# Optimization experiments

Hardware: AMD Instinct MI355X
Metric: run time of the kernel (lower is better)

Reference implementation:

```python
import jax, jax.numpy as jnp
import numpy as np

D_MODEL, SEQ, D_HEAD, N_HEAD, D_MLP = 1024, 2048, 64, 16, 4096
BATCH = 2
LN_EPS = 1e-5


def layer_norm(x, gamma, beta):
    mu = jnp.mean(x, axis=-1, keepdims=True)
    var = jnp.mean(jnp.square(x - mu), axis=-1, keepdims=True)
    return (x - mu) * jax.lax.rsqrt(var + LN_EPS) * gamma + beta


def setup_inputs() -> dict:
    key = jax.random.key(0)
    ks = jax.random.split(key, 10)
    s = 1.0 / np.sqrt(D_MODEL)
    x = jax.random.normal(ks[0], (BATCH, SEQ, D_MODEL), dtype=jnp.float32)
    # per-head Q/K/V projections, stacked: [H, d_model, d_head]
    wq = jax.random.uniform(ks[1], (N_HEAD, D_MODEL, D_HEAD), jnp.float32, -s, s)
    wk = jax.random.uniform(ks[2], (N_HEAD, D_MODEL, D_HEAD), jnp.float32, -s, s)
    wv = jax.random.uniform(ks[3], (N_HEAD, D_MODEL, D_HEAD), jnp.float32, -s, s)
    wo = jax.random.uniform(ks[4], (N_HEAD * D_HEAD, D_MODEL), jnp.float32, -s, s)
    sm = 1.0 / np.sqrt(D_MLP)
    w_in = jax.random.uniform(ks[5], (D_MODEL, D_MLP), jnp.float32, -s, s)
    b_in = jax.random.uniform(ks[6], (D_MLP,), jnp.float32, -s, s)
    w_out = jax.random.uniform(ks[7], (D_MLP, D_MODEL), jnp.float32, -sm, sm)
    b_out = jax.random.uniform(ks[8], (D_MODEL,), jnp.float32, -sm, sm)
    g1 = jnp.ones((D_MODEL,), jnp.float32)
    bt1 = jnp.zeros((D_MODEL,), jnp.float32)
    g2 = jnp.ones((D_MODEL,), jnp.float32)
    bt2 = jnp.zeros((D_MODEL,), jnp.float32)
    return {"x": x, "wq": wq, "wk": wk, "wv": wv, "wo": wo,
            "w_in": w_in, "b_in": b_in, "w_out": w_out, "b_out": b_out,
            "g1": g1, "bt1": bt1, "g2": g2, "bt2": bt2}


def reference(x, wq, wk, wv, wo, w_in, b_in, w_out, b_out, g1, bt1, g2, bt2):
    B, S, D = x.shape
    # multi-head attention (all heads batched)
    q = jnp.einsum('bsd,hde->bhse', x, wq)  # [B,H,S,dh]
    k = jnp.einsum('bsd,hde->bhse', x, wk)
    v = jnp.einsum('bsd,hde->bhse', x, wv)
    scores = jnp.einsum('bhie,bhje->bhij', q, k) / np.sqrt(D_HEAD)
    causal = jnp.tril(jnp.ones((S, S), dtype=bool))
    scores = jnp.where(causal, scores, -jnp.inf)
    attn = jax.nn.softmax(scores, axis=-1)
    head_out = jnp.einsum('bhij,bhje->bhie', attn, v)  # [B,H,S,dh]
    # concat heads in order (head 0 first) -> [B,S,H*dh]
    head_out = jnp.transpose(head_out, (0, 2, 1, 3)).reshape(B, S, N_HEAD * D_HEAD)
    x = x + layer_norm(head_out @ wo, g1, bt1)
    mlp = jax.nn.relu(x @ w_in + b_in) @ w_out + b_out
    x = x + layer_norm(mlp, g2, bt2)
    return x
```

## Files before the change

kernel.cpp:

```cpp
#include <hip/hip_runtime.h>
#include <hip/hip_bf16.h>
#include <math.h>

#define DM 1024
#define SEQ 2048
#define DH 64
#define NH 16
#define DMLP 4096
#define BATCH 2
#define ROWS (BATCH*SEQ)

typedef __attribute__((ext_vector_type(4))) float f32x4;
typedef __attribute__((ext_vector_type(8))) short bf16x8;

__device__ __forceinline__ void gl2lds16(const __hip_bfloat16* g, __hip_bfloat16* l) {
  __builtin_amdgcn_global_load_lds(
      (const __attribute__((address_space(1))) void*)g,
      (__attribute__((address_space(3))) void*)l, 16, 0, 0);
}

__device__ __forceinline__ float bfu2f(unsigned short u) {
  union { unsigned int i; float f; } cvt;
  cvt.i = ((unsigned int)u) << 16;
  return cvt.f;
}

template<int K, int OUT_BF16, int BIAS, int RELU>
__global__ __launch_bounds__(512) void gemm256(
    const __hip_bfloat16* __restrict__ A,
    const __hip_bfloat16* __restrict__ BT,
    float* __restrict__ Cf,
    __hip_bfloat16* __restrict__ Cb,
    const float* __restrict__ bias,
    int N)
{
  constexpr int NT = K / 64;
  __shared__ __align__(16) __hip_bfloat16 As[2][16384];
  __shared__ __align__(16) __hip_bfloat16 Bs[2][16384];
  const int t    = threadIdx.x;
  const int wave = t >> 6;
  const int lane = t & 63;
  const int col  = lane & 15;
  const int quad = lane >> 4;
  const int m0 = blockIdx.x * 256;
  const int n0 = blockIdx.y * 256;
  const int wm = (wave >> 2) * 128;
  const int wn = (wave & 3) * 64;

  const int tr = t >> 3;
  const int tc = (t & 7) ^ (tr & 7);
  const __hip_bfloat16* gA = A  + (size_t)(m0 + tr) * K + tc * 8;
  const __hip_bfloat16* gB = BT + (size_t)(n0 + tr) * K + tc * 8;

  const int sw  = col & 7;
  const int ao0 = ((quad)     ^ sw) * 8;
  const int ao1 = ((4 + quad) ^ sw) * 8;

  f32x4 acc[8][4] = {};

#define STAGE_A(h, u) do {                                                     \
    gl2lds16(gA + (size_t)(h)*128*K + (u)*64,                                  \
             &As[(u)&1][(h)*8192 + wave*512]);                                 \
    gl2lds16(gA + (size_t)(h)*128*K + (u)*64 + (size_t)64*K,                   \
             &As[(u)&1][(h)*8192 + 4096 + wave*512]);                          \
  } while (0)
#define STAGE_B(h, u) do {                                                     \
    gl2lds16(gB + (size_t)(h)*128*K + (u)*64,                                  \
             &Bs[(u)&1][(h)*8192 + wave*512]);                                 \
    gl2lds16(gB + (size_t)(h)*128*K + (u)*64 + (size_t)64*K,                   \
             &Bs[(u)&1][(h)*8192 + 4096 + wave*512]);                          \
  } while (0)
#define LOAD_A(base) do { _Pragma("unroll")                                    \
    for (int i = 0; i < 4; ++i) {                                              \
      af[i][0] = *(const bf16x8*)(pA + (base) + i*1024 + ao0);                 \
      af[i][1] = *(const bf16x8*)(pA + (base) + i*1024 + ao1);                 \
    } } while (0)
#define LOAD_BX(arr, base) do { _Pragma("unroll")                              \
    for (int j = 0; j < 2; ++j) {                                              \
      arr[j][0] = *(const bf16x8*)(pB + (base) + j*1024 + ao0);                \
      arr[j][1] = *(const bf16x8*)(pB + (base) + j*1024 + ao1);                \
    } } while (0)
#define PHASE_TAIL(MB, NB, BARR) do {                                          \
    asm volatile("s_barrier" ::: "memory");                                    \
    asm volatile("s_waitcnt lgkmcnt(0)" ::: "memory");                         \
    __builtin_amdgcn_s_setprio(1);                                             \
    _Pragma("unroll")                                                          \
    for (int kk = 0; kk < 2; ++kk)                                             \
      _Pragma("unroll")                                                        \
      for (int i = 0; i < 4; ++i)                                              \
        _Pragma("unroll")                                                      \
        for (int j = 0; j < 2; ++j)                                            \
          acc[(MB)+i][(NB)+j] = __builtin_amdgcn_mfma_f32_16x16x32_bf16(       \
              af[i][kk], BARR[j][kk], acc[(MB)+i][(NB)+j], 0, 0, 0);           \
    __builtin_amdgcn_s_setprio(0);                                             \
    asm volatile("s_barrier" ::: "memory");                                    \
  } while (0)

  STAGE_A(0, 0); STAGE_B(0, 0); STAGE_A(1, 0); STAGE_B(1, 0);
  if (NT > 1) {
    STAGE_A(0, 1); STAGE_B(0, 1); STAGE_A(1, 1); STAGE_B(1, 1);
    asm volatile("s_waitcnt vmcnt(8)" ::: "memory");
  } else {
    asm volatile("s_waitcnt vmcnt(0)" ::: "memory");
  }
  asm volatile("s_barrier" ::: "memory");

  #pragma unroll 2
  for (int u = 0; u < NT; ++u) {
    const __hip_bfloat16* pA = As[u & 1] + (wm + col) * 64;
    const __hip_bfloat16* pB = Bs[u & 1] + (wn + col) * 64;
    const bool s2 = (u + 2 < NT);
    bf16x8 af[4][2], bl[2][2], bh[2][2];

    LOAD_A(0);
    LOAD_BX(bl, 0);
    PHASE_TAIL(0, 0, bl);

    LOAD_BX(bh, 2048);
    PHASE_TAIL(0, 2, bh);

    LOAD_A(4096);
    if (s2) { STAGE_B(0, u + 2); STAGE_B(1, u + 2); }
    PHASE_TAIL(4, 2, bh);

    if (s2) {
      STAGE_A(0, u + 2); STAGE_A(1, u + 2);
      asm volatile("s_waitcnt vmcnt(8)" ::: "memory");
    } else {
      asm volatile("s_waitcnt vmcnt(0)" ::: "memory");
    }
    PHASE_TAIL(4, 0, bl);
  }
#undef STAGE_A
#undef STAGE_B
#undef LOAD_A
#undef LOAD_BX
#undef PHASE_TAIL

  #pragma unroll
  for (int mi = 0; mi < 8; ++mi) {
    #pragma unroll
    for (int ni = 0; ni < 4; ++ni) {
      const int cn = n0 + wn + ni*16 + col;
      float bv = 0.f;
      if (BIAS) bv = bias[cn];
      #pragma unroll
      for (int r = 0; r < 4; ++r) {
        const int cm = m0 + wm + mi*16 + quad*4 + r;
        float v = acc[mi][ni][r];
        if (BIAS) v += bv;
        if (RELU) v = fmaxf(v, 0.f);
        if (OUT_BF16) Cb[(size_t)cm * N + cn] = __float2bfloat16(v);
        else          Cf[(size_t)cm * N + cn] = v;
      }
    }
  }
}

template<int KS>
__global__ __launch_bounds__(512) void gemm256x128(
    const __hip_bfloat16* __restrict__ A,
    const __hip_bfloat16* __restrict__ BT,
    float* __restrict__ Cf,
    int N, int K, long long zstride)
{
  constexpr int NT = KS / 64;
  static_assert(NT >= 2, "pipeline needs >=2 K-tiles");
  __shared__ __align__(16) __hip_bfloat16 As[2][16384];
  __shared__ __align__(16) __hip_bfloat16 Bs[2][8192];
  const int t    = threadIdx.x;
  const int wave = t >> 6;
  const int lane = t & 63;
  const int col  = lane & 15;
  const int quad = lane >> 4;
  const int m0 = blockIdx.x * 256;
  const int n0 = blockIdx.y * 128;
  const int kz = (int)blockIdx.z * KS;
  const int wm = (wave >> 1) * 64;
  const int wn = (wave & 1) * 64;

  const int tr = t >> 3;
  const int tc = (t & 7) ^ (tr & 7);
  const __hip_bfloat16* gA = A  + (size_t)(m0 + tr) * K + kz + tc * 8;
  const __hip_bfloat16* gB = BT + (size_t)(n0 + tr) * K + kz + tc * 8;

  const int sw  = col & 7;
  const int ao0 = ((quad)     ^ sw) * 8;
  const int ao1 = ((4 + quad) ^ sw) * 8;

  f32x4 acc[4][4] = {};

#define SA(u) do { _Pragma("unroll")                                           \
    for (int q = 0; q < 4; ++q)                                                \
      gl2lds16(gA + (size_t)(q*64)*K + (u)*64,                                 \
               &As[(u)&1][q*4096 + wave*512]);                                 \
  } while (0)
#define SB(u) do { _Pragma("unroll")                                           \
    for (int q = 0; q < 2; ++q)                                                \
      gl2lds16(gB + (size_t)(q*64)*K + (u)*64,                                 \
               &Bs[(u)&1][q*4096 + wave*512]);                                 \
  } while (0)

  SA(0); SB(0); SA(1);

  #pragma unroll 2
  for (int v = 0; v < NT; ++v) {
    const __hip_bfloat16* pA = As[v & 1] + (wm + col) * 64;
    const __hip_bfloat16* pB = Bs[v & 1] + (wn + col) * 64;
    bf16x8 af[4][2], bf[4][2];

    if (v + 1 < NT) {
      SB(v + 1);
      asm volatile("s_waitcnt vmcnt(6)" ::: "memory");
    } else {
      asm volatile("s_waitcnt vmcnt(0)" ::: "memory");
    }
    asm volatile("s_barrier" ::: "memory");
    #pragma unroll
    for (int i = 0; i < 4; ++i) {
      af[i][0] = *(const bf16x8*)(pA + i*1024 + ao0);
      af[i][1] = *(const bf16x8*)(pA + i*1024 + ao1);
    }
    #pragma unroll
    for (int j = 0; j < 2; ++j) {
      bf[j][0] = *(const bf16x8*)(pB + j*1024 + ao0);
      bf[j][1] = *(const bf16x8*)(pB + j*1024 + ao1);
    }
    asm volatile("s_waitcnt lgkmcnt(0)" ::: "memory");
    __builtin_amdgcn_s_setprio(1);
    #pragma unroll
    for (int kk = 0; kk < 2; ++kk)
      #pragma unroll
      for (int i = 0; i < 4; ++i)
        #pragma unroll
        for (int j = 0; j < 2; ++j)
          acc[i][j] = __builtin_amdgcn_mfma_f32_16x16x32_bf16(
              af[i][kk], bf[j][kk], acc[i][j], 0, 0, 0);
    __builtin_amdgcn_s_setprio(0);
    asm volatile("s_barrier" ::: "memory");

    if (v + 2 < NT) SA(v + 2);
    #pragma unroll
    for (int j = 2; j < 4; ++j) {
      bf[j][0] = *(const bf16x8*)(pB + j*1024 + ao0);
      bf[j][1] = *(const bf16x8*)(pB + j*1024 + ao1);
    }
    asm volatile("s_waitcnt lgkmcnt(0)" ::: "memory");
    __builtin_amdgcn_s_setprio(1);
    #pragma unroll
    for (int kk = 0; kk < 2; ++kk)
      #pragma unroll
      for (int i = 0; i < 4; ++i)
        #pragma unroll
        for (int j = 2; j < 4; ++j)
          acc[i][j] = __builtin_amdgcn_mfma_f32_16x16x32_bf16(
              af[i][kk], bf[j][kk], acc[i][j], 0, 0, 0);
    __builtin_amdgcn_s_setprio(0);
    asm volatile("s_barrier" ::: "memory");
  }
#undef SA
#undef SB

  float* Co = Cf + (size_t)blockIdx.z * zstride;
  #pragma unroll
  for (int i = 0; i < 4; ++i) {
    #pragma unroll
    for (int j = 0; j < 4; ++j) {
      const int cn = n0 + wn + j*16 + col;
      #pragma unroll
      for (int r = 0; r < 4; ++r) {
        const int cm = m0 + wm + i*16 + quad*4 + r;
        Co[(size_t)cm * N + cn] = acc[i][j][r];
      }
    }
  }
}

__global__ __launch_bounds__(256) void attn_kernel(
    const __hip_bfloat16* __restrict__ qkv,
    const __hip_bfloat16* __restrict__ vt,
    __hip_bfloat16* __restrict__ aout,
    __hip_bfloat16* __restrict__ opart,
    float* __restrict__ lpart)
{
  __shared__ __align__(16) __hip_bfloat16 Ks[2][64*64];
  __shared__ __align__(16) __hip_bfloat16 Vts[2][64*64];
  __shared__ __align__(16) __hip_bfloat16 Ps[4][16*64];

  const int bh = blockIdx.x, b = bh >> 4, h = bh & 15;
  const int t = threadIdx.x, wave = t >> 6, lane = t & 63;
  const int col = lane & 15, quad = lane >> 4;
  const float SC = 0.125f * 1.44269504f;

  const int r0  = t >> 3;
  const int cs0 = (t & 7) ^ (r0 & 7);
  const __hip_bfloat16* kbase = qkv + (size_t)b*SEQ*3072 + 1024 + h*64;
  const __hip_bfloat16* vbase = vt + (size_t)bh*64*SEQ;

#define KISSUE(j0, buf) do {                                                      \
    gl2lds16(kbase + (size_t)((j0) + r0)*3072      + cs0*8, &Ks[buf][wave*512]);  \
    gl2lds16(kbase + (size_t)((j0) + 32 + r0)*3072 + cs0*8, &Ks[buf][2048 + wave*512]); \
  } while (0)
#define VISSUE(j0, buf) do {                                                      \
    gl2lds16(vbase + (size_t)r0*SEQ        + (j0) + cs0*8,  &Vts[buf][wave*512]); \
    gl2lds16(vbase + (size_t)(32 + r0)*SEQ + (j0) + cs0*8,  &Vts[buf][2048 + wave*512]); \
  } while (0)

  const int y = (int)blockIdx.y;
  int c, tile;
  if (y < 32)      { c = 0; tile = 31 - y;  }
  else if (y < 56) { c = 1; tile = 63 - y;  }
  else if (y < 72) { c = 2; tile = 87 - y;  }
  else             { c = 3; tile = 103 - y; }
  const int jbeg = c * 8;
  const int jend = jbeg + min(8, tile + 1 - jbeg);

  const int i0 = tile * 64;
  const int i0w = i0 + wave*16;

  bf16x8 aq[2];
  #pragma unroll
  for (int kk = 0; kk < 2; kk++)
    aq[kk] = *(const bf16x8*)&qkv[((size_t)(b*SEQ + i0w + col))*3072 + h*64 + kk*32 + quad*8];

  f32x4 O[4] = {};
  float lsum[4] = {0.f, 0.f, 0.f, 0.f};

  KISSUE(jbeg * 64, 0);
  VISSUE(jbeg * 64, 0);
  for (int jt = jbeg; jt < jend; jt++) {
    const int cur = (jt - jbeg) & 1;
    const int j0 = jt * 64;
    const bool pf = (jt + 1 < jend);
    asm volatile("s_barrier" ::: "memory");
    if (pf) {
      KISSUE(j0 + 64, cur ^ 1);
      VISSUE(j0 + 64, cur ^ 1);
      asm volatile("s_waitcnt vmcnt(4)" ::: "memory");
    } else {
      asm volatile("s_waitcnt vmcnt(0)" ::: "memory");
    }

    f32x4 S[4] = {};
    __builtin_amdgcn_s_setprio(1);
    #pragma unroll
    for (int kk = 0; kk < 2; kk++) {
      const int sl = ((kk*4 + quad) ^ (col & 7)) * 8;
      #pragma unroll
      for (int jl = 0; jl < 4; jl++) {
        bf16x8 bk = *(const bf16x8*)&Ks[cur][(jl*16 + col)*64 + sl];
        S[jl] = __builtin_amdgcn_mfma_f32_16x16x32_bf16(aq[kk], bk, S[jl], 0, 0, 0);
      }
    }
    __builtin_amdgcn_s_setprio(0);

    if (jt == tile) {
      #pragma unroll
      for (int r = 0; r < 4; r++) {
        const int row = quad*4 + r;
        const int ig = i0 + wave*16 + row;
        #pragma unroll
        for (int jl = 0; jl < 4; jl++) {
          float p = __builtin_amdgcn_exp2f(S[jl][r] * SC);
          if (j0 + jl*16 + col > ig) p = 0.f;
          lsum[r] += p;
          const int cc = jl*2 + (col >> 3);
          Ps[wave][row*64 + (cc ^ (row & 7))*8 + (col & 7)] = __float2bfloat16(p);
        }
      }
    } else {
      #pragma unroll
      for (int r = 0; r < 4; r++) {
        const int row = quad*4 + r;
        #pragma unroll
        for (int jl = 0; jl < 4; jl++) {
          float p = __builtin_amdgcn_exp2f(S[jl][r] * SC);
          lsum[r] += p;
          const int cc = jl*2 + (col >> 3);
          Ps[wave][row*64 + (cc ^ (row & 7))*8 + (col & 7)] = __float2bfloat16(p);
        }
      }
    }

    __builtin_amdgcn_s_setprio(1);
    #pragma unroll
    for (int kk = 0; kk < 2; kk++) {
      const int sl = ((kk*4 + quad) ^ (col & 7)) * 8;
      bf16x8 ap = *(const bf16x8*)&Ps[wave][col*64 + sl];
      #pragma unroll
      for (int et = 0; et < 4; et++) {
        bf16x8 bv = *(const bf16x8*)&Vts[cur][(et*16 + col)*64 + sl];
        O[et] = __builtin_amdgcn_mfma_f32_16x16x32_bf16(ap, bv, O[et], 0, 0, 0);
      }
    }
    __builtin_amdgcn_s_setprio(0);
  }

  #pragma unroll
  for (int r = 0; r < 4; r++) {
    float s = lsum[r];
    s += __shfl_xor(s, 1);
    s += __shfl_xor(s, 2);
    s += __shfl_xor(s, 4);
    s += __shfl_xor(s, 8);
    const int m = b*SEQ + i0w + quad*4 + r;
    if (tile < 8) {
      const float inv = __builtin_amdgcn_rcpf(s);
      #pragma unroll
      for (int et = 0; et < 4; et++)
        aout[(size_t)m*DM + h*64 + et*16 + col] = __float2bfloat16(O[et][r] * inv);
    } else {
      __hip_bfloat16* op = opart + ((size_t)c*ROWS + m)*DM + h*64;
      #pragma unroll
      for (int et = 0; et < 4; et++)
        op[et*16 + col] = __float2bfloat16(O[et][r]);
      if (col == 0) lpart[((size_t)c*ROWS + m)*16 + h] = s;
    }
  }
#undef KISSUE
#undef VISSUE
}

__global__ __launch_bounds__(256) void attn_finalize(
    const __hip_bfloat16* __restrict__ opart,
    const float* __restrict__ lpart,
    __hip_bfloat16* __restrict__ aout)
{
  const int y = blockIdx.x;
  const int b = y / 1536;
  const int rem = y % 1536;
  const int tile = 8 + (rem >> 6);
  const int rr = rem & 63;
  const int m = b*SEQ + tile*64 + rr;
  const int nch = (tile >> 3) + 1;
  const int tid = threadIdx.x;
  const int h = tid >> 4;
  float o0 = 0.f, o1 = 0.f, o2 = 0.f, o3 = 0.f, l = 0.f;
  for (int c = 0; c < nch; ++c) {
    const ushort4 v = ((const ushort4*)(opart + ((size_t)c*ROWS + m)*DM))[tid];
    o0 += bfu2f(v.x); o1 += bfu2f(v.y); o2 += bfu2f(v.z); o3 += bfu2f(v.w);
    l  += lpart[((size_t)c*ROWS + m)*16 + h];
  }
  const float inv = __builtin_amdgcn_rcpf(l);
  __hip_bfloat16* p = aout + (size_t)m*DM + tid*4;
  p[0] = __float2bfloat16(o0 * inv);
  p[1] = __float2bfloat16(o1 * inv);
  p[2] = __float2bfloat16(o2 * inv);
  p[3] = __float2bfloat16(o3 * inv);
}

__global__ __launch_bounds__(256) void ln_res(
    const float* __restrict__ y0,
    const float* __restrict__ y1,
    const float* __restrict__ bias,
    const float* __restrict__ xres,
    float* __restrict__ xout,
    __hip_bfloat16* __restrict__ bout,
    const float* __restrict__ gamma,
    const float* __restrict__ beta)
{
  const int row = blockIdx.x;
  const int t = threadIdx.x;
  float4 v = ((const float4*)(y0 + (size_t)row*DM))[t];
  if (y1) {
    const float4 w = ((const float4*)(y1 + (size_t)row*DM))[t];
    v.x += w.x; v.y += w.y; v.z += w.z; v.w += w.w;
  }
  if (bias) {
    const float4 w = ((const float4*)bias)[t];
    v.x += w.x; v.y += w.y; v.z += w.z; v.w += w.w;
  }
  float s  = v.x + v.y + v.z + v.w;
  float sq = v.x*v.x + v.y*v.y + v.z*v.z + v.w*v.w;
  #pragma unroll
  for (int off = 32; off > 0; off >>= 1) {
    s  += __shfl_down(s, off);
    sq += __shfl_down(sq, off);
  }
  __shared__ float red[8];
  const int wave = t >> 6, lane = t & 63;
  if (lane == 0) { red[wave] = s; red[4 + wave] = sq; }
  __syncthreads();
  s  = red[0] + red[1] + red[2] + red[3];
  sq = red[4] + red[5] + red[6] + red[7];
  const float mu   = s * (1.f/DM);
  const float var  = sq * (1.f/DM) - mu*mu;
  const float rstd = rsqrtf(var + 1e-5f);
  const float4 g  = ((const float4*)gamma)[t];
  const float4 bt = ((const float4*)beta)[t];
  const float4 xr = ((const float4*)(xres + (size_t)row*DM))[t];
  float4 o;
  o.x = (v.x - mu)*rstd*g.x + bt.x + xr.x;
  o.y = (v.y - mu)*rstd*g.y + bt.y + xr.y;
  o.z = (v.z - mu)*rstd*g.z + bt.z + xr.z;
  o.w = (v.w - mu)*rstd*g.w + bt.w + xr.w;
  ((float4*)(xout + (size_t)row*DM))[t] = o;
  if (bout) {
    __hip_bfloat16* bp = bout + (size_t)row*DM + t*4;
    bp[0] = __float2bfloat16(o.x);
    bp[1] = __float2bfloat16(o.y);
    bp[2] = __float2bfloat16(o.z);
    bp[3] = __float2bfloat16(o.w);
  }
}

__global__ __launch_bounds__(256) void transpose_cvt(
    const float* __restrict__ src, __hip_bfloat16* __restrict__ dst,
    int K, int N, long long sz, long long dz)
{
  __shared__ float tile[32][33];
  const int z = blockIdx.z;
  const int k0 = blockIdx.y * 32, n0 = blockIdx.x * 32;
  const int tx = threadIdx.x & 31, ty = threadIdx.x >> 5;
  const float* s = src + (size_t)z*sz;
  __hip_bfloat16* d = dst + (size_t)z*dz;
  for (int i = ty; i < 32; i += 8)
    tile[i][tx] = s[(size_t)(k0+i)*N + n0 + tx];
  __syncthreads();
  for (int i = ty; i < 32; i += 8)
    d[(size_t)(n0+i)*K + k0 + tx] = __float2bfloat16(tile[tx][i]);
}

__global__ __launch_bounds__(256) void transpose_v(
    const __hip_bfloat16* __restrict__ qkv, __hip_bfloat16* __restrict__ vt)
{
  __shared__ __hip_bfloat16 tile[32][33];
  const int bh = blockIdx.z, b = bh >> 4, h = bh & 15;
  const int s0 = blockIdx.x * 32, e0 = blockIdx.y * 32;
  const int tx = threadIdx.x & 31, ty = threadIdx.x >> 5;
  for (int i = ty; i < 32; i += 8)
    tile[i][tx] = qkv[(size_t)(b*SEQ + s0+i)*3072 + 2048 + h*64 + e0 + tx];
  __syncthreads();
  for (int i = ty; i < 32; i += 8)
    vt[((size_t)bh*64 + e0+i)*SEQ + s0 + tx] = tile[tx][i];
}

__global__ __launch_bounds__(256) void cvt_bf16(
    const float* __restrict__ src, __hip_bfloat16* __restrict__ dst, int n4)
{
  const int i = blockIdx.x*256 + threadIdx.x;
  if (i < n4) {
    const float4 v = ((const float4*)src)[i];
    dst[i*4+0] = __float2bfloat16(v.x);
    dst[i*4+1] = __float2bfloat16(v.y);
    dst[i*4+2] = __float2bfloat16(v.z);
    dst[i*4+3] = __float2bfloat16(v.w);
  }
}

extern "C" void kernel_launch(void* const* d_in, const int* in_sizes, int n_in,
                              void* d_out, int out_size, void* d_ws, size_t ws_size,
                              hipStream_t stream)
{
  const float* x     = (const float*)d_in[0];
  const float* wq    = (const float*)d_in[1];
  const float* wk    = (const float*)d_in[2];
  const float* wv    = (const float*)d_in[3];
  const float* wo    = (const float*)d_in[4];
  const float* w_in  = (const float*)d_in[5];
  const float* b_in  = (const float*)d_in[6];
  const float* w_out = (const float*)d_in[7];
  const float* b_out = (const float*)d_in[8];
  const float* g1    = (const float*)d_in[9];
  const float* bt1   = (const float*)d_in[10];
  const float* g2    = (const float*)d_in[11];
  const float* bt2   = (const float*)d_in[12];
  float* out = (float*)d_out;

  char* ws = (char*)d_ws;
  __hip_bfloat16* xb     = (__hip_bfloat16*)(ws + 0);
  __hip_bfloat16* wqkvT  = (__hip_bfloat16*)(ws + 8388608);
  __hip_bfloat16* woT    = (__hip_bfloat16*)(ws + 14680064);
  __hip_bfloat16* w_inT  = (__hip_bfloat16*)(ws + 16777216);
  __hip_bfloat16* w_outT = (__hip_bfloat16*)(ws + 25165824);
  __hip_bfloat16* qkvb   = (__hip_bfloat16*)(ws + 33554432);
  __hip_bfloat16* vtb    = (__hip_bfloat16*)(ws + 58720256);
  __hip_bfloat16* attn_o = (__hip_bfloat16*)(ws + 0);
  __hip_bfloat16* opart  = (__hip_bfloat16*)(ws + 67108864);
  float*          lpart  = (float*)(ws + 100663296);
  float*          P0     = (float*)(ws + 33554432);
  float*          x1     = (float*)(ws + 75497472);
  __hip_bfloat16* x1b    = (__hip_bfloat16*)(ws + 92274688);
  __hip_bfloat16* hbuf   = (__hip_bfloat16*)(ws + 33554432);
  float*          M0     = (float*)(ws + 0);
  float*          M1     = (float*)(ws + 100663296);
  float*          P1     = (float*)(ws + 50331648);

  const long long PROJ_ZS = (long long)ROWS * DM;
  const long long MLP_ZS  = 100663296LL / 4;

  cvt_bf16<<<ROWS*DM/4/256, 256, 0, stream>>>(x, xb, ROWS*DM/4);

  transpose_cvt<<<dim3(2,32,16), 256, 0, stream>>>(wq, wqkvT,             DM, DH, (long long)DM*DH, (long long)DH*DM);
  transpose_cvt<<<dim3(2,32,16), 256, 0, stream>>>(wk, wqkvT + 1024*1024, DM, DH, (long long)DM*DH, (long long)DH*DM);
  transpose_cvt<<<dim3(2,32,16), 256, 0, stream>>>(wv, wqkvT + 2048*1024, DM, DH, (long long)DM*DH, (long long)DH*DM);
  transpose_cvt<<<dim3(32,32,1),  256, 0, stream>>>(wo,    woT,    DM,   DM,   0, 0);
  transpose_cvt<<<dim3(128,32,1), 256, 0, stream>>>(w_in,  w_inT,  DM,   DMLP, 0, 0);
  transpose_cvt<<<dim3(32,128,1), 256, 0, stream>>>(w_out, w_outT, DMLP, DM,   0, 0);

  gemm256<DM,1,0,0><<<dim3(ROWS/256, 3072/256), 512, 0, stream>>>(xb, wqkvT, nullptr, qkvb, nullptr, 3072);
  transpose_v<<<dim3(SEQ/32, 2, BATCH*NH), 256, 0, stream>>>(qkvb, vtb);
  attn_kernel<<<dim3(BATCH*NH, 80), 256, 0, stream>>>(qkvb, vtb, attn_o, opart, lpart);
  attn_finalize<<<3072, 256, 0, stream>>>(opart, lpart, attn_o);
  gemm256x128<512><<<dim3(ROWS/256, DM/128, 2), 512, 0, stream>>>(attn_o, woT, P0, DM, DM, PROJ_ZS);
  ln_res<<<ROWS, 256, 0, stream>>>(P0, P1, nullptr, x, x1, x1b, g1, bt1);
  gemm256<DM,1,1,1><<<dim3(ROWS/256, DMLP/256), 512, 0, stream>>>(x1b, w_inT, nullptr, hbuf, b_in, DMLP);
  gemm256x128<2048><<<dim3(ROWS/256, DM/128, 2), 512, 0, stream>>>(hbuf, w_outT, M0, DM, DMLP, MLP_ZS);
  ln_res<<<ROWS, 256, 0, stream>>>(M0, M1, b_out, x1, out, nullptr, g2, bt2);
}
```

Before: 233.5 us.

## Double attention query tile to 128 rows per block with transposed score layout

Each attention block now processes 128 query rows (32 per wave, two 16-row sub-tiles), so every K/V tile staged in LDS is reused for twice as many queries and the grid halves. The MFMA operands are swapped so scores come out transposed, which lets P be written to LDS as packed 4-element vectors and outputs stored as ushort4. The split-KV chunking and the finalize indexing are remapped to the 128-row tiles. The cost is more registers per wave, fewer blocks to balance across CUs, and extra masked work on diagonal tiles.

```diff
diff --git a/kernel.cpp b/kernel.cpp
--- a/kernel.cpp
+++ b/kernel.cpp
@@ -23,6 +23,11 @@
   union { unsigned int i; float f; } cvt;
   cvt.i = ((unsigned int)u) << 16;
   return cvt.f;
+}
+
+__device__ __forceinline__ unsigned short f2bu(float f) {
+  __hip_bfloat16 h = __float2bfloat16(f);
+  return *reinterpret_cast<unsigned short*>(&h);
 }
 
 template<int K, int OUT_BF16, int BIAS, int RELU>
@@ -285,7 +290,7 @@
 {
   __shared__ __align__(16) __hip_bfloat16 Ks[2][64*64];
   __shared__ __align__(16) __hip_bfloat16 Vts[2][64*64];
-  __shared__ __align__(16) __hip_bfloat16 Ps[4][16*64];
+  __shared__ __align__(16) __hip_bfloat16 PsT[8][16*64];
 
   const int bh = blockIdx.x, b = bh >> 4, h = bh & 15;
   const int t = threadIdx.x, wave = t >> 6, lane = t & 63;
@@ -307,24 +312,29 @@
   } while (0)
 
   const int y = (int)blockIdx.y;
-  int c, tile;
-  if (y < 32)      { c = 0; tile = 31 - y;  }
-  else if (y < 56) { c = 1; tile = 63 - y;  }
-  else if (y < 72) { c = 2; tile = 87 - y;  }
-  else             { c = 3; tile = 103 - y; }
+  int c, tl;
+  if (y < 16)      { c = 0; tl = 15 - y; }
+  else if (y < 28) { c = 1; tl = 31 - y; }
+  else if (y < 36) { c = 2; tl = 43 - y; }
+  else             { c = 3; tl = 51 - y; }
   const int jbeg = c * 8;
-  const int jend = jbeg + min(8, tile + 1 - jbeg);
-
-  const int i0 = tile * 64;
-  const int i0w = i0 + wave*16;
-
-  bf16x8 aq[2];
+  const int njt  = 2*tl + 2;
+  const int jend = min(jbeg + 8, njt);
+
+  const int i0 = tl * 128;
+  const int iw = i0 + wave*32;
+
+  bf16x8 aq[2][2];
   #pragma unroll
-  for (int kk = 0; kk < 2; kk++)
-    aq[kk] = *(const bf16x8*)&qkv[((size_t)(b*SEQ + i0w + col))*3072 + h*64 + kk*32 + quad*8];
-
-  f32x4 O[4] = {};
-  float lsum[4] = {0.f, 0.f, 0.f, 0.f};
+  for (int ib = 0; ib < 2; ib++)
+    #pragma unroll
+    for (int kk = 0; kk < 2; kk++)
+      aq[ib][kk] = *(const bf16x8*)&qkv[((size_t)(b*SEQ + iw + ib*16 + col))*3072 + h*64 + kk*32 + quad*8];
+
+  f32x4 O[4][2] = {};
+  float lsum[2] = {0.f, 0.f};
+
+  const int swj = (col & 7) << 3;
 
   KISSUE(jbeg * 64, 0);
   VISSUE(jbeg * 64, 0);
@@ -341,7 +351,7 @@
       asm volatile("s_waitcnt vmcnt(0)" ::: "memory");
     }
 
-    f32x4 S[4] = {};
+    f32x4 S[4][2] = {};
     __builtin_amdgcn_s_setprio(1);
     #pragma unroll
     for (int kk = 0; kk < 2; kk++) {
@@ -349,72 +359,87 @@
       #pragma unroll
       for (int jl = 0; jl < 4; jl++) {
         bf16x8 bk = *(const bf16x8*)&Ks[cur][(jl*16 + col)*64 + sl];
-        S[jl] = __builtin_amdgcn_mfma_f32_16x16x32_bf16(aq[kk], bk, S[jl], 0, 0, 0);
+        #pragma unroll
+        for (int ib = 0; ib < 2; ib++)
+          S[jl][ib] = __builtin_amdgcn_mfma_f32_16x16x32_bf16(bk, aq[ib][kk], S[jl][ib], 0, 0, 0);
       }
     }
     __builtin_amdgcn_s_setprio(0);
 
-    if (jt == tile) {
-      #pragma unroll
-      for (int r = 0; r < 4; r++) {
-        const int row = quad*4 + r;
-        const int ig = i0 + wave*16 + row;
+    #pragma unroll
+    for (int ib = 0; ib < 2; ib++) {
+      const int ig = iw + ib*16 + col;
+      if (j0 + 64 > iw + ib*16) {
         #pragma unroll
         for (int jl = 0; jl < 4; jl++) {
-          float p = __builtin_amdgcn_exp2f(S[jl][r] * SC);
-          if (j0 + jl*16 + col > ig) p = 0.f;
-          lsum[r] += p;
-          const int cc = jl*2 + (col >> 3);
-          Ps[wave][row*64 + (cc ^ (row & 7))*8 + (col & 7)] = __float2bfloat16(p);
+          float p[4];
+          #pragma unroll
+          for (int r = 0; r < 4; r++) {
+            float v = __builtin_amdgcn_exp2f(S[jl][ib][r] * SC);
+            if (j0 + jl*16 + quad*4 + r > ig) v = 0.f;
+            p[r] = v;
+            lsum[ib] += v;
+          }
+          ushort4 pk = { f2bu(p[0]), f2bu(p[1]), f2bu(p[2]), f2bu(p[3]) };
+          *(ushort4*)&PsT[wave*2 + ib][col*64 + ((jl*16 + quad*4) ^ swj)] = pk;
+        }
+      } else {
+        #pragma unroll
+        for (int jl = 0; jl < 4; jl++) {
+          float p[4];
+          #pragma unroll
+          for (int r = 0; r < 4; r++) {
+            p[r] = __builtin_amdgcn_exp2f(S[jl][ib][r] * SC);
+            lsum[ib] += p[r];
+          }
+          ushort4 pk = { f2bu(p[0]), f2bu(p[1]), f2bu(p[2]), f2bu(p[3]) };
+          *(ushort4*)&PsT[wave*2 + ib][col*64 + ((jl*16 + quad*4) ^ swj)] = pk;
         }
       }
-    } else {
-      #pragma unroll
-      for (int r = 0; r < 4; r++) {
-        const int row = quad*4 + r;
-        #pragma unroll
-        for (int jl = 0; jl < 4; jl++) {
-          float p = __builtin_amdgcn_exp2f(S[jl][r] * SC);
-          lsum[r] += p;
-          const int cc = jl*2 + (col >> 3);
-          Ps[wave][row*64 + (cc ^ (row & 7))*8 + (col & 7)] = __float2bfloat16(p);
-        }
-      }
     }
 
     __builtin_amdgcn_s_setprio(1);
     #pragma unroll
     for (int kk = 0; kk < 2; kk++) {
       const int sl = ((kk*4 + quad) ^ (col & 7)) * 8;
-      bf16x8 ap = *(const bf16x8*)&Ps[wave][col*64 + sl];
+      bf16x8 ap[2];
+      #pragma unroll
+      for (int ib = 0; ib < 2; ib++)
+        ap[ib] = *(const bf16x8*)&PsT[wave*2 + ib][col*64 + ((kk*32 + quad*8) ^ swj)];
       #pragma unroll
       for (int et = 0; et < 4; et++) {
         bf16x8 bv = *(const bf16x8*)&Vts[cur][(et*16 + col)*64 + sl];
-        O[et] = __builtin_amdgcn_mfma_f32_16x16x32_bf16(ap, bv, O[et], 0, 0, 0);
+        #pragma unroll
+        for (int ib = 0; ib < 2; ib++)
+          O[et][ib] = __builtin_amdgcn_mfma_f32_16x16x32_bf16(bv, ap[ib], O[et][ib], 0, 0, 0);
       }
     }
     __builtin_amdgcn_s_setprio(0);
   }
 
   #pragma unroll
-  for (int r = 0; r < 4; r++) {
-    float s = lsum[r];
-    s += __shfl_xor(s, 1);
-    s += __shfl_xor(s, 2);
-    s += __shfl_xor(s, 4);
-    s += __shfl_xor(s, 8);
-    const int m = b*SEQ + i0w + quad*4 + r;
-    if (tile < 8) {
+  for (int ib = 0; ib < 2; ib++) {
+    float s = lsum[ib];
+    s += __shfl_xor(s, 16);
+    s += __shfl_xor(s, 32);
+    const int m = b*SEQ + iw + ib*16 + col;
+    if (tl < 4) {
       const float inv = __builtin_amdgcn_rcpf(s);
       #pragma unroll
-      for (int et = 0; et < 4; et++)
-        aout[(size_t)m*DM + h*64 + et*16 + col] = __float2bfloat16(O[et][r] * inv);
+      for (int et = 0; et < 4; et++) {
+        ushort4 o = { f2bu(O[et][ib][0]*inv), f2bu(O[et][ib][1]*inv),
+                      f2bu(O[et][ib][2]*inv), f2bu(O[et][ib][3]*inv) };
+        *(ushort4*)&aout[(size_t)m*DM + h*64 + et*16 + quad*4] = o;
+      }
     } else {
       __hip_bfloat16* op = opart + ((size_t)c*ROWS + m)*DM + h*64;
       #pragma unroll
-      for (int et = 0; et < 4; et++)
-        op[et*16 + col] = __float2bfloat16(O[et][r]);
-      if (col == 0) lpart[((size_t)c*ROWS + m)*16 + h] = s;
+      for (int et = 0; et < 4; et++) {
+        ushort4 o = { f2bu(O[et][ib][0]), f2bu(O[et][ib][1]),
+                      f2bu(O[et][ib][2]), f2bu(O[et][ib][3]) };
+        *(ushort4*)&op[et*16 + quad*4] = o;
+      }
+      if (quad == 0) lpart[((size_t)c*ROWS + m)*16 + h] = s;
     }
   }
 #undef KISSUE
@@ -429,10 +454,10 @@
   const int y = blockIdx.x;
   const int b = y / 1536;
   const int rem = y % 1536;
-  const int tile = 8 + (rem >> 6);
-  const int rr = rem & 63;
-  const int m = b*SEQ + tile*64 + rr;
-  const int nch = (tile >> 3) + 1;
+  const int tl = 4 + (rem >> 7);
+  const int rr = rem & 127;
+  const int m = b*SEQ + tl*128 + rr;
+  const int nch = (tl >> 2) + 1;
   const int tid = threadIdx.x;
   const int h = tid >> 4;
   float o0 = 0.f, o1 = 0.f, o2 = 0.f, o3 = 0.f, l = 0.f;
@@ -600,7 +625,7 @@
 
   gemm256<DM,1,0,0><<<dim3(ROWS/256, 3072/256), 512, 0, stream>>>(xb, wqkvT, nullptr, qkvb, nullptr, 3072);
   transpose_v<<<dim3(SEQ/32, 2, BATCH*NH), 256, 0, stream>>>(qkvb, vtb);
-  attn_kernel<<<dim3(BATCH*NH, 80), 256, 0, stream>>>(qkvb, vtb, attn_o, opart, lpart);
+  attn_kernel<<<dim3(BATCH*NH, 40), 256, 0, stream>>>(qkvb, vtb, attn_o, opart, lpart);
   attn_finalize<<<3072, 256, 0, stream>>>(opart, lpart, attn_o);
   gemm256x128<512><<<dim3(ROWS/256, DM/128, 2), 512, 0, stream>>>(attn_o, woT, P0, DM, DM, PROJ_ZS);
   ln_res<<<ROWS, 256, 0, stream>>>(P0, P1, nullptr, x, x1, x1b, g1, bt1);
```

New measurement: 233.0 us. No clear change (-0.2%).
